# Kernel optimization log

Hardware: AMD Instinct MI355X
Metric: run time of the kernel (lower is better)

The kernel has to match this reference:

```python
import jax, jax.numpy as jnp
import numpy as np

B, S, H, L = 4096, 64, 768, 5
TEMP = 0.07
BN_EPS = 1e-5


def setup_inputs() -> dict:
    key = jax.random.key(0)
    ks = jax.random.split(key, 8)
    seq = jax.random.normal(ks[0], (B, S, H), dtype=jnp.float32)
    labels = jax.random.randint(ks[1], (B,), 0, L)
    s = 1.0 / np.sqrt(H)
    return {
        'sequence_output': seq,
        'cls_gamma': jnp.ones((H,), jnp.float32),
        'cls_beta': jnp.zeros((H,), jnp.float32),
        'cls_W': jax.random.normal(ks[2], (H, H), jnp.float32) * s,
        'cls_b': jax.random.normal(ks[3], (H,), jnp.float32) * 0.01,
        'label_gamma': jnp.ones((H,), jnp.float32),
        'label_beta': jnp.zeros((H,), jnp.float32),
        'label_W': jax.random.normal(ks[4], (H, H), jnp.float32) * s,
        'label_b': jax.random.normal(ks[5], (H,), jnp.float32) * 0.01,
        'labels': labels,
    }


def _batchnorm(x, gamma, beta):
    # training-mode BatchNorm1d: biased batch stats
    m = x.mean(0)
    v = jnp.mean((x - m) ** 2, axis=0)
    return (x - m) * jax.lax.rsqrt(v + BN_EPS) * gamma + beta


def _l2norm(x):
    return x / jnp.sqrt(jnp.sum(x * x, axis=-1, keepdims=True)).clip(1e-12)


def reference(sequence_output, cls_gamma, cls_beta, cls_W, cls_b,
              label_gamma, label_beta, label_W, label_b, labels):
    z = sequence_output[:, 0, :]  # [B,H]; dropout is identity in eval
    # label token spans: 'No relation' -> positions 1:3 (mean), rest single tokens 3..6
    theta = jnp.stack([
        sequence_output[:, 1:3, :].mean(axis=1),
        sequence_output[:, 3, :],
        sequence_output[:, 4, :],
        sequence_output[:, 5, :],
        sequence_output[:, 6, :],
    ], axis=1)  # [B,L,H]
    z_cl, theta_cl = z, theta

    zp = _batchnorm(z, cls_gamma, cls_beta) @ cls_W.T + cls_b  # [B,H]
    tp = _batchnorm(theta.reshape(-1, H), label_gamma, label_beta) @ label_W.T + label_b
    tp = tp.reshape(-1, L, H)  # [B,L,H]
    logits = jnp.einsum('blh,bh->bl', tp, zp)  # [B,L]

    # ---- dual supervised contrastive loss (vectorized over the python loops) ----
    z_norm = _l2norm(z_cl)        # [B,H]
    theta_norm = _l2norm(theta_cl)  # [B,L,H]
    same = labels[:, None] == labels[None, :]          # [B,B]
    eye = jnp.eye(labels.shape[0], dtype=bool)
    pos_mask = (same & ~eye).astype(jnp.float32)       # positives (same label, j != i)
    neg_mask = (~same).astype(jnp.float32)             # negatives (different label)
    has_pos = (same & ~eye).any(axis=1)

    # l_z: anchor z_i vs theta_j[labels_i] (pos) and all theta_j[:] for diff-label j (neg)
    expS = jnp.exp(jnp.einsum('ih,jlh->ijl', z_norm, theta_norm) / TEMP)  # [B,B,L]
    expS_at_lab = jnp.take_along_axis(
        expS, jnp.broadcast_to(labels[:, None, None], expS.shape[:2] + (1,)), axis=2
    )[..., 0]  # expS[i,j,labels[i]] -> [B,B]
    pos_z = jnp.sum(expS_at_lab * pos_mask, axis=1)
    neg_z = jnp.sum(expS.sum(axis=-1) * neg_mask, axis=1)
    l_z = jnp.where(has_pos, -jnp.log(pos_z / (pos_z + neg_z + 1e-8)), 0.0).sum()

    # l_theta: anchor theta_i[labels_i] vs z_j
    anchor_theta = jnp.take_along_axis(theta_norm, labels[:, None, None], axis=1)[:, 0, :]  # [B,H]
    expT = jnp.exp(anchor_theta @ z_norm.T / TEMP)  # [B,B]
    pos_t = jnp.sum(expT * pos_mask, axis=1)
    neg_t = jnp.sum(expT * neg_mask, axis=1)
    l_t = jnp.where(has_pos, -jnp.log(pos_t / (pos_t + neg_t + 1e-8)), 0.0).sum()

    dual_loss = (l_z + l_t) / labels.shape[0]
    return logits, dual_loss
```

## Files before the change

### kernel.cpp

```cpp
#include <hip/hip_runtime.h>
#include <hip/hip_bf16.h>
#include <cstdint>
#include <cstddef>

#define B_N 4096
#define S_N 64
#define H_N 768
#define L_N 5
#define TEMP_INV (1.0f / 0.07f)
#define BN_EPS 1e-5f

typedef __attribute__((ext_vector_type(8))) short short8;
typedef __attribute__((ext_vector_type(4))) float f32x4;

__device__ __forceinline__ void async_copy16(void* lds, const void* g) {
  __builtin_amdgcn_global_load_lds(
      (const __attribute__((address_space(1))) unsigned int*)g,
      (__attribute__((address_space(3))) unsigned int*)lds, 16, 0, 0);
}

__device__ __forceinline__ unsigned short bf16b(float x) {
  __hip_bfloat16 h = __float2bfloat16(x);
  return *reinterpret_cast<unsigned short*>(&h);
}
__device__ __forceinline__ void store_bf16x4(void* p, float4 v) {
  ushort4 o = make_ushort4(bf16b(v.x), bf16b(v.y), bf16b(v.z), bf16b(v.w));
  *reinterpret_cast<ushort4*>(p) = o;
}

__device__ inline float block_reduce_sum256(float v, float* sbuf) {
#pragma unroll
  for (int off = 32; off > 0; off >>= 1) v += __shfl_down(v, off, 64);
  int lane = threadIdx.x & 63;
  int wid = threadIdx.x >> 6;
  __syncthreads();
  if (lane == 0) sbuf[wid] = v;
  __syncthreads();
  float r = 0.f;
  if (threadIdx.x == 0) r = sbuf[0] + sbuf[1] + sbuf[2] + sbuf[3];
  return r;
}

__global__ __launch_bounds__(256) void extract_kernel(
    const float* __restrict__ seq, __hip_bfloat16* __restrict__ zb,
    __hip_bfloat16* __restrict__ tb, float* __restrict__ zn_inv,
    float* __restrict__ thn_inv, float* __restrict__ sum_z,
    float* __restrict__ ssq_z, float* __restrict__ sum_t,
    float* __restrict__ ssq_t) {
  __shared__ float pr[8][6][3];
  int t = threadIdx.x;
  int wv = t >> 6, ln = t & 63;
  bool act = t < 192;
  int c4 = t * 4;
  int b0 = blockIdx.x * 8;
  float zs[4] = {}, zq[4] = {}, ts4[4] = {}, tq4[4] = {};
  for (int r = 0; r < 8; ++r) {
    int b = b0 + r;
    const float* base = seq + (size_t)b * (S_N * H_N);
    float pv[6] = {0.f, 0.f, 0.f, 0.f, 0.f, 0.f};
    if (act) {
      float4 z4 = *(const float4*)(base + c4);
      store_bf16x4(zb + (size_t)b * H_N + c4, z4);
      pv[0] = z4.x * z4.x + z4.y * z4.y + z4.z * z4.z + z4.w * z4.w;
      zs[0] += z4.x; zs[1] += z4.y; zs[2] += z4.z; zs[3] += z4.w;
      zq[0] += z4.x * z4.x; zq[1] += z4.y * z4.y;
      zq[2] += z4.z * z4.z; zq[3] += z4.w * z4.w;
#pragma unroll
      for (int l = 0; l < L_N; ++l) {
        float4 v4;
        if (l == 0) {
          float4 a4 = *(const float4*)(base + H_N + c4);
          float4 b4 = *(const float4*)(base + 2 * H_N + c4);
          v4 = make_float4(0.5f * (a4.x + b4.x), 0.5f * (a4.y + b4.y),
                           0.5f * (a4.z + b4.z), 0.5f * (a4.w + b4.w));
        } else {
          v4 = *(const float4*)(base + (size_t)(l + 2) * H_N + c4);
        }
        store_bf16x4(tb + ((size_t)b * L_N + l) * H_N + c4, v4);
        pv[1 + l] = v4.x * v4.x + v4.y * v4.y + v4.z * v4.z + v4.w * v4.w;
        ts4[0] += v4.x; ts4[1] += v4.y; ts4[2] += v4.z; ts4[3] += v4.w;
        tq4[0] += v4.x * v4.x; tq4[1] += v4.y * v4.y;
        tq4[2] += v4.z * v4.z; tq4[3] += v4.w * v4.w;
      }
    }
#pragma unroll
    for (int v = 0; v < 6; ++v) {
      float x = pv[v];
#pragma unroll
      for (int off = 32; off > 0; off >>= 1) x += __shfl_down(x, off, 64);
      if (ln == 0 && wv < 3) pr[r][v][wv] = x;
    }
  }
  __syncthreads();
  if (t < 48) {
    int r = t / 6, v = t - r * 6;
    float s = pr[r][v][0] + pr[r][v][1] + pr[r][v][2];
    float inv = 1.f / fmaxf(sqrtf(s), 1e-12f);
    int b = b0 + r;
    if (v == 0) zn_inv[b] = inv;
    else thn_inv[b * L_N + (v - 1)] = inv;
  }
  if (act) {
#pragma unroll
    for (int j = 0; j < 4; ++j) {
      atomicAdd(&sum_z[c4 + j], zs[j]);
      atomicAdd(&ssq_z[c4 + j], zq[j]);
      atomicAdd(&sum_t[c4 + j], ts4[j]);
      atomicAdd(&ssq_t[c4 + j], tq4[j]);
    }
  }
}

__global__ void count_kernel(const int* __restrict__ labels, int* __restrict__ cnt) {
  int i = blockIdx.x * 256 + threadIdx.x;
  if (i < B_N) atomicAdd(&cnt[labels[i]], 1);
}

__global__ void finalize_kernel(
    const float* __restrict__ sum_z, const float* __restrict__ ssq_z,
    const float* __restrict__ sum_t, const float* __restrict__ ssq_t,
    const float* __restrict__ g_z, const float* __restrict__ b_z,
    const float* __restrict__ g_t, const float* __restrict__ b_t,
    float* __restrict__ sz_s, float* __restrict__ sz_t,
    float* __restrict__ st_s, float* __restrict__ st_t) {
  int h = blockIdx.x * 256 + threadIdx.x;
  if (h >= H_N) return;
  {
    float m = sum_z[h] * (1.f / B_N);
    float v = ssq_z[h] * (1.f / B_N) - m * m;
    float s = g_z[h] * rsqrtf(v + BN_EPS);
    sz_s[h] = s;
    sz_t[h] = b_z[h] - m * s;
  }
  {
    float m = sum_t[h] * (1.f / (B_N * L_N));
    float v = ssq_t[h] * (1.f / (B_N * L_N)) - m * m;
    float s = g_t[h] * rsqrtf(v + BN_EPS);
    st_s[h] = s;
    st_t[h] = b_t[h] - m * s;
  }
}

__global__ __launch_bounds__(256) void prep_cls_kernel(
    const float* __restrict__ W, const float* __restrict__ szs,
    const float* __restrict__ szt, const float* __restrict__ bias,
    __hip_bfloat16* __restrict__ Wb, float* __restrict__ cprime) {
  __shared__ float sbuf[4];
  int n = blockIdx.x;
  int t = threadIdx.x;
  float dot = 0.f;
  if (t < 192) {
    int c4 = t * 4;
    const float* row = W + (size_t)n * H_N;
    float4 w4 = *(const float4*)(row + c4);
    float4 s4 = *(const float4*)(szs + c4);
    float4 t4 = *(const float4*)(szt + c4);
    store_bf16x4(Wb + (size_t)n * H_N + c4,
                 make_float4(w4.x * s4.x, w4.y * s4.y, w4.z * s4.z, w4.w * s4.w));
    dot = w4.x * t4.x + w4.y * t4.y + w4.z * t4.z + w4.w * t4.w;
  }
  float s = block_reduce_sum256(dot, sbuf);
  if (t == 0) cprime[n] = s + bias[n];
}

__global__ __launch_bounds__(256) void transpose_wl_kernel(
    const float* __restrict__ Wl, __hip_bfloat16* __restrict__ WlT) {
  __shared__ float tile[32][33];
  int t = threadIdx.x;
  int tx = t & 31, ty0 = t >> 5;
  int n0 = blockIdx.x * 32, k0 = blockIdx.y * 32;
#pragma unroll
  for (int p = 0; p < 4; ++p)
    tile[ty0 + p * 8][tx] = Wl[(size_t)(n0 + ty0 + p * 8) * H_N + k0 + tx];
  __syncthreads();
#pragma unroll
  for (int p = 0; p < 4; ++p) {
    unsigned short us = bf16b(tile[tx][ty0 + p * 8]);
    *((unsigned short*)WlT + (size_t)(k0 + ty0 + p * 8) * H_N + n0 + tx) = us;
  }
}

template <bool WRITE_BF16, bool HAS_BIAS>
__global__ __launch_bounds__(256) void gemm128_kernel(
    const __hip_bfloat16* __restrict__ A, const __hip_bfloat16* __restrict__ Bm,
    const float* __restrict__ bias, float* __restrict__ outF,
    __hip_bfloat16* __restrict__ outB) {
  __shared__ __align__(16) __hip_bfloat16 Asm[128 * 32];
  __shared__ __align__(16) __hip_bfloat16 Bsm[128 * 32];
  int tid = threadIdx.x, lane = tid & 63, wid = tid >> 6;
  int wr = wid >> 1, wc = wid & 1;
  int i0 = blockIdx.x * 128, n0 = blockIdx.y * 128;
  int llo = lane & 15, lhi = lane >> 4;
  f32x4 acc[4][4] = {};
  for (int k0 = 0; k0 < H_N; k0 += 32) {
#pragma unroll
    for (int r = 0; r < 2; ++r) {
      int s = r * 256 + wid * 64 + lane;
      int row = s >> 2, kc = (s & 3) * 8;
      size_t go = (size_t)row * H_N + k0 + kc;
      async_copy16((char*)Asm + (size_t)(r * 256 + wid * 64) * 16,
                   A + (size_t)i0 * H_N + go);
      async_copy16((char*)Bsm + (size_t)(r * 256 + wid * 64) * 16,
                   Bm + (size_t)n0 * H_N + go);
    }
    __syncthreads();
    short8 a[4], b[4];
#pragma unroll
    for (int m = 0; m < 4; ++m)
      a[m] = *(const short8*)((const char*)Asm +
                              ((wr * 64 + m * 16 + llo) * 32 + lhi * 8) * 2);
#pragma unroll
    for (int n = 0; n < 4; ++n)
      b[n] = *(const short8*)((const char*)Bsm +
                              ((wc * 64 + n * 16 + llo) * 32 + lhi * 8) * 2);
#pragma unroll
    for (int m = 0; m < 4; ++m)
#pragma unroll
      for (int n = 0; n < 4; ++n)
        acc[m][n] =
            __builtin_amdgcn_mfma_f32_16x16x32_bf16(a[m], b[n], acc[m][n], 0, 0, 0);
    __syncthreads();
  }
#pragma unroll
  for (int n = 0; n < 4; ++n) {
    int col = n0 + wc * 64 + n * 16 + llo;
    float bv = HAS_BIAS ? bias[col] : 0.f;
#pragma unroll
    for (int m = 0; m < 4; ++m) {
#pragma unroll
      for (int r = 0; r < 4; ++r) {
        int row = i0 + wr * 64 + m * 16 + lhi * 4 + r;
        float val = acc[m][n][r] + bv;
        outF[(size_t)row * H_N + col] = val;
        if (WRITE_BF16)
          outB[(size_t)row * H_N + col] = __float2bfloat16(val);
      }
    }
  }
}

__global__ __launch_bounds__(256) void logits_kernel(
    const float* __restrict__ seq, const float* __restrict__ u,
    const float* __restrict__ zp, const float* __restrict__ st_s,
    const float* __restrict__ st_t, const float* __restrict__ label_b,
    float* __restrict__ out) {
  __shared__ float sbuf[4];
  int b = blockIdx.x;
  int t = threadIdx.x;
  bool act = t < 192;
  int c4 = t * 4;
  float4 w4 = make_float4(0.f, 0.f, 0.f, 0.f);
  float apart = 0.f;
  if (act) {
    float4 u4 = *(const float4*)(u + (size_t)b * H_N + c4);
    float4 zp4 = *(const float4*)(zp + (size_t)b * H_N + c4);
    float4 ss4 = *(const float4*)(st_s + c4);
    float4 tt4 = *(const float4*)(st_t + c4);
    float4 lb4 = *(const float4*)(label_b + c4);
    w4 = make_float4(u4.x * ss4.x, u4.y * ss4.y, u4.z * ss4.z, u4.w * ss4.w);
    apart = u4.x * tt4.x + u4.y * tt4.y + u4.z * tt4.z + u4.w * tt4.w +
            zp4.x * lb4.x + zp4.y * lb4.y + zp4.z * lb4.z + zp4.w * lb4.w;
  }
  float alpha = block_reduce_sum256(apart, sbuf);
  const float* base = seq + (size_t)b * (S_N * H_N);
#pragma unroll
  for (int l = 0; l < L_N; ++l) {
    float part = 0.f;
    if (act) {
      float4 v4;
      if (l == 0) {
        float4 a4 = *(const float4*)(base + H_N + c4);
        float4 b4 = *(const float4*)(base + 2 * H_N + c4);
        v4 = make_float4(0.5f * (a4.x + b4.x), 0.5f * (a4.y + b4.y),
                         0.5f * (a4.z + b4.z), 0.5f * (a4.w + b4.w));
      } else {
        v4 = *(const float4*)(base + (size_t)(l + 2) * H_N + c4);
      }
      part = v4.x * w4.x + v4.y * w4.y + v4.z * w4.z + v4.w * w4.w;
    }
    float s = block_reduce_sum256(part, sbuf);
    if (t == 0) out[b * L_N + l] = s + alpha;
  }
}

#define NT_K 24
__global__ __launch_bounds__(256, 3) void sgemm_fused_kernel(
    const __hip_bfloat16* __restrict__ zb, const __hip_bfloat16* __restrict__ tb,
    const float* __restrict__ zn_inv, const float* __restrict__ thn_inv,
    const int* __restrict__ labels, float* __restrict__ pos_z,
    float* __restrict__ neg_z, float* __restrict__ pos_t,
    float* __restrict__ neg_t) {
  __shared__ __align__(128) char ldsbuf[2][16384];

  const int tid = threadIdx.x;
  const int lane = tid & 63, wid = tid >> 6;
  const int llo = lane & 15, lhi = lane >> 4;
  const int wr = wid >> 1, wc = wid & 1;
  const int xcd = blockIdx.x & 7;
  const int s0 = blockIdx.x >> 3;
  const int i0 = (xcd * 4 + (s0 & 3)) * 128;
  const int n0 = (s0 >> 2) * 128;

  f32x4 acc[4][4] = {};

  auto stage = [&](int c, int kt) {
#pragma unroll
    for (int h = 0; h < 2; ++h) {
      int s = h * 256 + tid;
      int R = s >> 3, sp = s & 7;
      int l = sp ^ (R & 7);
      int grow = 2 * R + (l >> 2);
      int gk = kt * 32 + (l & 3) * 8;
      int wub = (h * 256 + wid * 64) * 16;
      async_copy16(&ldsbuf[c][0] + wub, zb + (size_t)(i0 + grow) * H_N + gk);
      async_copy16(&ldsbuf[c][8192] + wub, tb + (size_t)(n0 + grow) * H_N + gk);
    }
  };

  auto fragOff = [&](int r) {
    int R = r >> 1;
    int slot = (r & 1) * 4 + lhi;
    return R * 128 + ((slot ^ (R & 7)) * 16);
  };

  stage(0, 0);
  asm volatile("s_waitcnt vmcnt(0)" ::: "memory");
  __builtin_amdgcn_s_barrier();

  for (int t = 0; t < NT_K; ++t) {
    if (t + 1 < NT_K) stage((t + 1) & 1, t + 1);
    const char* A = &ldsbuf[t & 1][0];
    const char* B = &ldsbuf[t & 1][8192];
    short8 a[4], b[4];
#pragma unroll
    for (int m = 0; m < 4; ++m) a[m] = *(const short8*)(A + fragOff(wr * 64 + m * 16 + llo));
#pragma unroll
    for (int n = 0; n < 4; ++n) b[n] = *(const short8*)(B + fragOff(wc * 64 + n * 16 + llo));
    asm volatile("s_waitcnt lgkmcnt(0)" ::: "memory");
    __builtin_amdgcn_sched_barrier(0);
    __builtin_amdgcn_s_setprio(1);
#pragma unroll
    for (int m = 0; m < 4; ++m)
#pragma unroll
      for (int n = 0; n < 4; ++n)
        acc[m][n] =
            __builtin_amdgcn_mfma_f32_16x16x32_bf16(a[m], b[n], acc[m][n], 0, 0, 0);
    __builtin_amdgcn_s_setprio(0);
    asm volatile("s_waitcnt vmcnt(0)" ::: "memory");
    __builtin_amdgcn_s_barrier();
  }
  __syncthreads();

  float* rpos = (float*)&ldsbuf[0][0];
  float* rneg = rpos + 128;
  float* cpos = rneg + 128;
  float* cneg = cpos + 128;
  float* rnorm = cneg + 128;
  float* cnorm = rnorm + 128;
  int* rowlab = (int*)(cnorm + 128);
  int* colj = rowlab + 128;
  int* coll = colj + 128;
  int* collab = coll + 128;

  if (tid < 128) {
    rowlab[tid] = labels[i0 + tid];
    rnorm[tid] = zn_inv[i0 + tid] * TEMP_INV;
    int c = n0 + tid;
    int j = c / 5;
    colj[tid] = j;
    coll[tid] = c - j * 5;
    collab[tid] = labels[j];
    cnorm[tid] = thn_inv[c];
    rpos[tid] = 0.f; rneg[tid] = 0.f; cpos[tid] = 0.f; cneg[tid] = 0.f;
  }
  __syncthreads();

  int cl[4], jg[4], lv[4], lj[4];
  float cs[4];
#pragma unroll
  for (int ni = 0; ni < 4; ++ni) {
    cl[ni] = wc * 64 + ni * 16 + llo;
    jg[ni] = colj[cl[ni]];
    lv[ni] = coll[cl[ni]];
    lj[ni] = collab[cl[ni]];
    cs[ni] = cnorm[cl[ni]];
  }
  float cpAcc[4] = {}, cnAcc[4] = {};
#pragma unroll
  for (int mi = 0; mi < 4; ++mi) {
#pragma unroll
    for (int r = 0; r < 4; ++r) {
      int rl = wr * 64 + mi * 16 + lhi * 4 + r;
      int ig = i0 + rl;
      int li = rowlab[rl];
      float rscale = rnorm[rl];
      float rp = 0.f, rn = 0.f;
#pragma unroll
      for (int ni = 0; ni < 4; ++ni) {
        float e = __expf(acc[mi][ni][r] * rscale * cs[ni]);
        bool same = (li == lj[ni]);
        bool diag = (ig == jg[ni]);
        if (same) {
          if (!diag && lv[ni] == li) { rp += e; cpAcc[ni] += e; }
        } else {
          rn += e;
          if (lv[ni] == lj[ni]) cnAcc[ni] += e;
        }
      }
      if (rp != 0.f) atomicAdd(&rpos[rl], rp);
      if (rn != 0.f) atomicAdd(&rneg[rl], rn);
    }
  }
#pragma unroll
  for (int ni = 0; ni < 4; ++ni) {
    if (cpAcc[ni] != 0.f) atomicAdd(&cpos[cl[ni]], cpAcc[ni]);
    if (cnAcc[ni] != 0.f) atomicAdd(&cneg[cl[ni]], cnAcc[ni]);
  }
  __syncthreads();
  if (tid < 128) {
    float v;
    v = rpos[tid]; if (v != 0.f) atomicAdd(&pos_z[i0 + tid], v);
    v = rneg[tid]; if (v != 0.f) atomicAdd(&neg_z[i0 + tid], v);
    int j = colj[tid];
    v = cpos[tid]; if (v != 0.f) atomicAdd(&pos_t[j], v);
    v = cneg[tid]; if (v != 0.f) atomicAdd(&neg_t[j], v);
  }
}

__global__ __launch_bounds__(256) void loss_kernel(
    const float* __restrict__ pos_z, const float* __restrict__ neg_z,
    const float* __restrict__ pos_t, const float* __restrict__ neg_t,
    const int* __restrict__ labels, const int* __restrict__ cnt,
    float* __restrict__ out_loss) {
  __shared__ float sbuf[4];
  int i = blockIdx.x * 256 + threadIdx.x;
  float term = 0.f;
  int li = labels[i];
  if (cnt[li] > 1) {
    float pz = pos_z[i], nz = neg_z[i];
    float pt = pos_t[i], nt = neg_t[i];
    term = -logf(pz / (pz + nz + 1e-8f)) - logf(pt / (pt + nt + 1e-8f));
  }
  float s = block_reduce_sum256(term, sbuf);
  if (threadIdx.x == 0) atomicAdd(out_loss, s * (1.0f / B_N));
}

extern "C" void kernel_launch(void* const* d_in, const int* in_sizes, int n_in,
                              void* d_out, int out_size, void* d_ws, size_t ws_size,
                              hipStream_t stream) {
  const float* seq = (const float*)d_in[0];
  const float* cls_gamma = (const float*)d_in[1];
  const float* cls_beta = (const float*)d_in[2];
  const float* cls_W = (const float*)d_in[3];
  const float* cls_b = (const float*)d_in[4];
  const float* label_gamma = (const float*)d_in[5];
  const float* label_beta = (const float*)d_in[6];
  const float* label_W = (const float*)d_in[7];
  const float* label_b = (const float*)d_in[8];
  const int* labels = (const int*)d_in[9];
  float* out = (float*)d_out;
  float* ws = (float*)d_ws;

  constexpr size_t OFF_SUMZ = 0;
  constexpr size_t OFF_SSQZ = 768;
  constexpr size_t OFF_SUMT = 1536;
  constexpr size_t OFF_SSQT = 2304;
  constexpr size_t OFF_POSZ = 3072;
  constexpr size_t OFF_NEGZ = 7168;
  constexpr size_t OFF_POST = 11264;
  constexpr size_t OFF_NEGT = 15360;
  constexpr size_t OFF_CNT = 19456;
  constexpr size_t ZERO_FLOATS = 19464;
  constexpr size_t OFF_SZS = 19464;
  constexpr size_t OFF_SZT = 20232;
  constexpr size_t OFF_STS = 21000;
  constexpr size_t OFF_STT = 21768;
  constexpr size_t OFF_ZNI = 22536;
  constexpr size_t OFF_TNI = 26632;
  constexpr size_t OFF_CPRIME = 47112;
  constexpr size_t OFF_ZP = 47880;
  constexpr size_t OFF_U = OFF_ZP + (size_t)B_N * H_N;
  constexpr size_t F32_END = OFF_U + (size_t)B_N * H_N;
  constexpr size_t BYTE_ZB = F32_END * sizeof(float);
  constexpr size_t BYTE_TB = BYTE_ZB + (size_t)B_N * H_N * 2;
  constexpr size_t BYTE_ZPB = BYTE_TB + (size_t)B_N * L_N * H_N * 2;
  constexpr size_t BYTE_WCB = BYTE_ZPB + (size_t)B_N * H_N * 2;
  constexpr size_t BYTE_WLT = BYTE_WCB + (size_t)H_N * H_N * 2;
  constexpr size_t TOTAL_BYTES = BYTE_WLT + (size_t)H_N * H_N * 2;
  if (ws_size < TOTAL_BYTES) return;

  __hip_bfloat16* zb = (__hip_bfloat16*)((char*)d_ws + BYTE_ZB);
  __hip_bfloat16* tb = (__hip_bfloat16*)((char*)d_ws + BYTE_TB);
  __hip_bfloat16* zpb = (__hip_bfloat16*)((char*)d_ws + BYTE_ZPB);
  __hip_bfloat16* wcb = (__hip_bfloat16*)((char*)d_ws + BYTE_WCB);
  __hip_bfloat16* wlt = (__hip_bfloat16*)((char*)d_ws + BYTE_WLT);

  hipMemsetAsync(d_ws, 0, ZERO_FLOATS * sizeof(float), stream);
  hipMemsetAsync((char*)d_out + (size_t)B_N * L_N * sizeof(float), 0, sizeof(float),
                 stream);

  extract_kernel<<<512, 256, 0, stream>>>(seq, zb, tb, ws + OFF_ZNI, ws + OFF_TNI,
                                          ws + OFF_SUMZ, ws + OFF_SSQZ,
                                          ws + OFF_SUMT, ws + OFF_SSQT);
  count_kernel<<<16, 256, 0, stream>>>(labels, (int*)(ws + OFF_CNT));
  finalize_kernel<<<3, 256, 0, stream>>>(
      ws + OFF_SUMZ, ws + OFF_SSQZ, ws + OFF_SUMT, ws + OFF_SSQT, cls_gamma,
      cls_beta, label_gamma, label_beta, ws + OFF_SZS, ws + OFF_SZT, ws + OFF_STS,
      ws + OFF_STT);
  prep_cls_kernel<<<H_N, 256, 0, stream>>>(cls_W, ws + OFF_SZS, ws + OFF_SZT, cls_b,
                                           wcb, ws + OFF_CPRIME);
  transpose_wl_kernel<<<dim3(24, 24), 256, 0, stream>>>(label_W, wlt);
  gemm128_kernel<true, true><<<dim3(32, 6), 256, 0, stream>>>(
      zb, wcb, ws + OFF_CPRIME, ws + OFF_ZP, zpb);
  gemm128_kernel<false, false><<<dim3(32, 6), 256, 0, stream>>>(
      zpb, wlt, nullptr, ws + OFF_U, nullptr);
  logits_kernel<<<B_N, 256, 0, stream>>>(seq, ws + OFF_U, ws + OFF_ZP, ws + OFF_STS,
                                         ws + OFF_STT, label_b, out);
  sgemm_fused_kernel<<<5120, 256, 0, stream>>>(
      zb, tb, ws + OFF_ZNI, ws + OFF_TNI, labels, ws + OFF_POSZ, ws + OFF_NEGZ,
      ws + OFF_POST, ws + OFF_NEGT);
  loss_kernel<<<16, 256, 0, stream>>>(ws + OFF_POSZ, ws + OFF_NEGZ, ws + OFF_POST,
                                      ws + OFF_NEGT, labels,
                                      (const int*)(ws + OFF_CNT),
                                      out + (size_t)B_N * L_N);
}
```

Baseline: 461.1 us.

## Load GEMM fragments directly from global into registers, dropping LDS staging

The bf16 similarity GEMM no longer stages tiles in LDS through async global-to-LDS copies with barriers. Each wave now loads its MFMA fragments straight from global memory into registers, double-buffered across two k-steps, and LDS is kept only for the small epilogue arrays. This removes the LDS round trip and the per-iteration barriers. In exchange, every wave re-fetches rows that other waves in the block also read, which raises global/L2 traffic, and the 16-byte loads per row are less coalesced.

```diff
diff --git a/kernel.cpp b/kernel.cpp
--- a/kernel.cpp
+++ b/kernel.cpp
@@ -290,7 +290,9 @@
     const int* __restrict__ labels, float* __restrict__ pos_z,
     float* __restrict__ neg_z, float* __restrict__ pos_t,
     float* __restrict__ neg_t) {
-  __shared__ __align__(128) char ldsbuf[2][16384];
+  __shared__ float rpos[128], rneg[128], cpos[128], cneg[128];
+  __shared__ float rnorm[128], cnorm[128];
+  __shared__ int rowlab[128], colj[128], coll[128], collab[128];
 
   const int tid = threadIdx.x;
   const int lane = tid & 63, wid = tid >> 6;
@@ -301,66 +303,47 @@
   const int i0 = (xcd * 4 + (s0 & 3)) * 128;
   const int n0 = (s0 >> 2) * 128;
 
+  const __hip_bfloat16* pa = zb + (size_t)(i0 + wr * 64 + llo) * H_N + lhi * 8;
+  const __hip_bfloat16* pb = tb + (size_t)(n0 + wc * 64 + llo) * H_N + lhi * 8;
+
   f32x4 acc[4][4] = {};
-
-  auto stage = [&](int c, int kt) {
-#pragma unroll
-    for (int h = 0; h < 2; ++h) {
-      int s = h * 256 + tid;
-      int R = s >> 3, sp = s & 7;
-      int l = sp ^ (R & 7);
-      int grow = 2 * R + (l >> 2);
-      int gk = kt * 32 + (l & 3) * 8;
-      int wub = (h * 256 + wid * 64) * 16;
-      async_copy16(&ldsbuf[c][0] + wub, zb + (size_t)(i0 + grow) * H_N + gk);
-      async_copy16(&ldsbuf[c][8192] + wub, tb + (size_t)(n0 + grow) * H_N + gk);
-    }
-  };
-
-  auto fragOff = [&](int r) {
-    int R = r >> 1;
-    int slot = (r & 1) * 4 + lhi;
-    return R * 128 + ((slot ^ (R & 7)) * 16);
-  };
-
-  stage(0, 0);
-  asm volatile("s_waitcnt vmcnt(0)" ::: "memory");
-  __builtin_amdgcn_s_barrier();
-
-  for (int t = 0; t < NT_K; ++t) {
-    if (t + 1 < NT_K) stage((t + 1) & 1, t + 1);
-    const char* A = &ldsbuf[t & 1][0];
-    const char* B = &ldsbuf[t & 1][8192];
-    short8 a[4], b[4];
-#pragma unroll
-    for (int m = 0; m < 4; ++m) a[m] = *(const short8*)(A + fragOff(wr * 64 + m * 16 + llo));
-#pragma unroll
-    for (int n = 0; n < 4; ++n) b[n] = *(const short8*)(B + fragOff(wc * 64 + n * 16 + llo));
-    asm volatile("s_waitcnt lgkmcnt(0)" ::: "memory");
-    __builtin_amdgcn_sched_barrier(0);
+  short8 a0[4], b0[4], a1[4], b1[4];
+
+#pragma unroll
+  for (int m = 0; m < 4; ++m) a0[m] = *(const short8*)(pa + m * 16 * H_N);
+#pragma unroll
+  for (int n = 0; n < 4; ++n) b0[n] = *(const short8*)(pb + n * 16 * H_N);
+
+  for (int t = 0; t < NT_K; t += 2) {
+    const int k1 = (t + 1) * 32;
+#pragma unroll
+    for (int m = 0; m < 4; ++m) a1[m] = *(const short8*)(pa + m * 16 * H_N + k1);
+#pragma unroll
+    for (int n = 0; n < 4; ++n) b1[n] = *(const short8*)(pb + n * 16 * H_N + k1);
     __builtin_amdgcn_s_setprio(1);
 #pragma unroll
     for (int m = 0; m < 4; ++m)
 #pragma unroll
       for (int n = 0; n < 4; ++n)
         acc[m][n] =
-            __builtin_amdgcn_mfma_f32_16x16x32_bf16(a[m], b[n], acc[m][n], 0, 0, 0);
+            __builtin_amdgcn_mfma_f32_16x16x32_bf16(a0[m], b0[n], acc[m][n], 0, 0, 0);
     __builtin_amdgcn_s_setprio(0);
-    asm volatile("s_waitcnt vmcnt(0)" ::: "memory");
-    __builtin_amdgcn_s_barrier();
-  }
-  __syncthreads();
-
-  float* rpos = (float*)&ldsbuf[0][0];
-  float* rneg = rpos + 128;
-  float* cpos = rneg + 128;
-  float* cneg = cpos + 128;
-  float* rnorm = cneg + 128;
-  float* cnorm = rnorm + 128;
-  int* rowlab = (int*)(cnorm + 128);
-  int* colj = rowlab + 128;
-  int* coll = colj + 128;
-  int* collab = coll + 128;
+    if (t + 2 < NT_K) {
+      const int k2 = (t + 2) * 32;
+#pragma unroll
+      for (int m = 0; m < 4; ++m) a0[m] = *(const short8*)(pa + m * 16 * H_N + k2);
+#pragma unroll
+      for (int n = 0; n < 4; ++n) b0[n] = *(const short8*)(pb + n * 16 * H_N + k2);
+    }
+    __builtin_amdgcn_s_setprio(1);
+#pragma unroll
+    for (int m = 0; m < 4; ++m)
+#pragma unroll
+      for (int n = 0; n < 4; ++n)
+        acc[m][n] =
+            __builtin_amdgcn_mfma_f32_16x16x32_bf16(a1[m], b1[n], acc[m][n], 0, 0, 0);
+    __builtin_amdgcn_s_setprio(0);
+  }
 
   if (tid < 128) {
     rowlab[tid] = labels[i0 + tid];
```

Measured after the change: 629.1 us. +36.4%, slower.

## Per-wave private LDS staging in contrastive GEMM, reuse bf16 theta in logits, fuse label count

Applied to the files above, without the earlier changes.

The fused contrastive GEMM now gives each wave its own LDS region holding only its 64-row A and B slices, triple-staged two tiles ahead. Each wave waits only on its own loads with vmcnt, so the per-iteration block barriers go away. LDS use doubles to 64KB and the occupancy hint of 3 is dropped, which may lower occupancy, and each wave now loads redundant copies of data its neighbours also load. Separately, logits reads the bf16 theta buffer instead of re-reading fp32 sequence rows, and the label-count kernel is folded into extract; the bf16 read slightly lowers logits precision.

```diff
diff --git a/kernel.cpp b/kernel.cpp
--- a/kernel.cpp
+++ b/kernel.cpp
@@ -27,6 +27,10 @@
   ushort4 o = make_ushort4(bf16b(v.x), bf16b(v.y), bf16b(v.z), bf16b(v.w));
   *reinterpret_cast<ushort4*>(p) = o;
 }
+__device__ __forceinline__ float bf2f(unsigned short u) {
+  unsigned int x = ((unsigned int)u) << 16;
+  return *reinterpret_cast<float*>(&x);
+}
 
 __device__ inline float block_reduce_sum256(float v, float* sbuf) {
 #pragma unroll
@@ -46,13 +50,15 @@
     __hip_bfloat16* __restrict__ tb, float* __restrict__ zn_inv,
     float* __restrict__ thn_inv, float* __restrict__ sum_z,
     float* __restrict__ ssq_z, float* __restrict__ sum_t,
-    float* __restrict__ ssq_t) {
+    float* __restrict__ ssq_t, const int* __restrict__ labels,
+    int* __restrict__ cnt) {
   __shared__ float pr[8][6][3];
   int t = threadIdx.x;
   int wv = t >> 6, ln = t & 63;
   bool act = t < 192;
   int c4 = t * 4;
   int b0 = blockIdx.x * 8;
+  if (t < 8) atomicAdd(&cnt[labels[b0 + t]], 1);
   float zs[4] = {}, zq[4] = {}, ts4[4] = {}, tq4[4] = {};
   for (int r = 0; r < 8; ++r) {
     int b = b0 + r;
@@ -109,11 +115,6 @@
       atomicAdd(&ssq_t[c4 + j], tq4[j]);
     }
   }
-}
-
-__global__ void count_kernel(const int* __restrict__ labels, int* __restrict__ cnt) {
-  int i = blockIdx.x * 256 + threadIdx.x;
-  if (i < B_N) atomicAdd(&cnt[labels[i]], 1);
 }
 
 __global__ void finalize_kernel(
@@ -240,7 +241,7 @@
 }
 
 __global__ __launch_bounds__(256) void logits_kernel(
-    const float* __restrict__ seq, const float* __restrict__ u,
+    const __hip_bfloat16* __restrict__ tb, const float* __restrict__ u,
     const float* __restrict__ zp, const float* __restrict__ st_s,
     const float* __restrict__ st_t, const float* __restrict__ label_b,
     float* __restrict__ out) {
@@ -262,21 +263,14 @@
             zp4.x * lb4.x + zp4.y * lb4.y + zp4.z * lb4.z + zp4.w * lb4.w;
   }
   float alpha = block_reduce_sum256(apart, sbuf);
-  const float* base = seq + (size_t)b * (S_N * H_N);
 #pragma unroll
   for (int l = 0; l < L_N; ++l) {
     float part = 0.f;
     if (act) {
-      float4 v4;
-      if (l == 0) {
-        float4 a4 = *(const float4*)(base + H_N + c4);
-        float4 b4 = *(const float4*)(base + 2 * H_N + c4);
-        v4 = make_float4(0.5f * (a4.x + b4.x), 0.5f * (a4.y + b4.y),
-                         0.5f * (a4.z + b4.z), 0.5f * (a4.w + b4.w));
-      } else {
-        v4 = *(const float4*)(base + (size_t)(l + 2) * H_N + c4);
-      }
-      part = v4.x * w4.x + v4.y * w4.y + v4.z * w4.z + v4.w * w4.w;
+      ushort4 tv = *(const ushort4*)((const unsigned short*)tb +
+                                     ((size_t)b * L_N + l) * H_N + c4);
+      part = bf2f(tv.x) * w4.x + bf2f(tv.y) * w4.y + bf2f(tv.z) * w4.z +
+             bf2f(tv.w) * w4.w;
     }
     float s = block_reduce_sum256(part, sbuf);
     if (t == 0) out[b * L_N + l] = s + alpha;
@@ -284,13 +278,13 @@
 }
 
 #define NT_K 24
-__global__ __launch_bounds__(256, 3) void sgemm_fused_kernel(
+__global__ __launch_bounds__(256) void sgemm_fused_kernel(
     const __hip_bfloat16* __restrict__ zb, const __hip_bfloat16* __restrict__ tb,
     const float* __restrict__ zn_inv, const float* __restrict__ thn_inv,
     const int* __restrict__ labels, float* __restrict__ pos_z,
     float* __restrict__ neg_z, float* __restrict__ pos_t,
     float* __restrict__ neg_t) {
-  __shared__ __align__(128) char ldsbuf[2][16384];
+  __shared__ __align__(128) char ldsbuf[4][16384];
 
   const int tid = threadIdx.x;
   const int lane = tid & 63, wid = tid >> 6;
@@ -301,19 +295,32 @@
   const int i0 = (xcd * 4 + (s0 & 3)) * 128;
   const int n0 = (s0 >> 2) * 128;
 
+  char* wbase = &ldsbuf[wid][0];
+  const __hip_bfloat16* srcA = zb + (size_t)(i0 + wr * 64) * H_N;
+  const __hip_bfloat16* srcB = tb + (size_t)(n0 + wc * 64) * H_N;
+
   f32x4 acc[4][4] = {};
 
   auto stage = [&](int c, int kt) {
-#pragma unroll
-    for (int h = 0; h < 2; ++h) {
-      int s = h * 256 + tid;
+    char* dA = wbase + c * 8192;
+    char* dB = dA + 4096;
+#pragma unroll
+    for (int i = 0; i < 4; ++i) {
+      int s = i * 64 + lane;
       int R = s >> 3, sp = s & 7;
       int l = sp ^ (R & 7);
       int grow = 2 * R + (l >> 2);
       int gk = kt * 32 + (l & 3) * 8;
-      int wub = (h * 256 + wid * 64) * 16;
-      async_copy16(&ldsbuf[c][0] + wub, zb + (size_t)(i0 + grow) * H_N + gk);
-      async_copy16(&ldsbuf[c][8192] + wub, tb + (size_t)(n0 + grow) * H_N + gk);
+      async_copy16(dA + i * 1024, srcA + (size_t)grow * H_N + gk);
+    }
+#pragma unroll
+    for (int i = 0; i < 4; ++i) {
+      int s = i * 64 + lane;
+      int R = s >> 3, sp = s & 7;
+      int l = sp ^ (R & 7);
+      int grow = 2 * R + (l >> 2);
+      int gk = kt * 32 + (l & 3) * 8;
+      async_copy16(dB + i * 1024, srcB + (size_t)grow * H_N + gk);
     }
   };
 
@@ -324,20 +331,22 @@
   };
 
   stage(0, 0);
-  asm volatile("s_waitcnt vmcnt(0)" ::: "memory");
-  __builtin_amdgcn_s_barrier();
-
+  stage(1, 1);
   for (int t = 0; t < NT_K; ++t) {
-    if (t + 1 < NT_K) stage((t + 1) & 1, t + 1);
-    const char* A = &ldsbuf[t & 1][0];
-    const char* B = &ldsbuf[t & 1][8192];
+    if (t < NT_K - 1)
+      asm volatile("s_waitcnt vmcnt(8)" ::: "memory");
+    else
+      asm volatile("s_waitcnt vmcnt(0)" ::: "memory");
+    const char* A = wbase + (t & 1) * 8192;
+    const char* B = A + 4096;
     short8 a[4], b[4];
 #pragma unroll
-    for (int m = 0; m < 4; ++m) a[m] = *(const short8*)(A + fragOff(wr * 64 + m * 16 + llo));
-#pragma unroll
-    for (int n = 0; n < 4; ++n) b[n] = *(const short8*)(B + fragOff(wc * 64 + n * 16 + llo));
+    for (int m = 0; m < 4; ++m) a[m] = *(const short8*)(A + fragOff(m * 16 + llo));
+#pragma unroll
+    for (int n = 0; n < 4; ++n) b[n] = *(const short8*)(B + fragOff(n * 16 + llo));
     asm volatile("s_waitcnt lgkmcnt(0)" ::: "memory");
     __builtin_amdgcn_sched_barrier(0);
+    if (t + 2 < NT_K) stage(t & 1, t + 2);
     __builtin_amdgcn_s_setprio(1);
 #pragma unroll
     for (int m = 0; m < 4; ++m)
@@ -346,8 +355,6 @@
         acc[m][n] =
             __builtin_amdgcn_mfma_f32_16x16x32_bf16(a[m], b[n], acc[m][n], 0, 0, 0);
     __builtin_amdgcn_s_setprio(0);
-    asm volatile("s_waitcnt vmcnt(0)" ::: "memory");
-    __builtin_amdgcn_s_barrier();
   }
   __syncthreads();
 
@@ -501,8 +508,8 @@
 
   extract_kernel<<<512, 256, 0, stream>>>(seq, zb, tb, ws + OFF_ZNI, ws + OFF_TNI,
                                           ws + OFF_SUMZ, ws + OFF_SSQZ,
-                                          ws + OFF_SUMT, ws + OFF_SSQT);
-  count_kernel<<<16, 256, 0, stream>>>(labels, (int*)(ws + OFF_CNT));
+                                          ws + OFF_SUMT, ws + OFF_SSQT, labels,
+                                          (int*)(ws + OFF_CNT));
   finalize_kernel<<<3, 256, 0, stream>>>(
       ws + OFF_SUMZ, ws + OFF_SSQZ, ws + OFF_SUMT, ws + OFF_SSQT, cls_gamma,
       cls_beta, label_gamma, label_beta, ws + OFF_SZS, ws + OFF_SZT, ws + OFF_STS,
@@ -514,7 +521,7 @@
       zb, wcb, ws + OFF_CPRIME, ws + OFF_ZP, zpb);
   gemm128_kernel<false, false><<<dim3(32, 6), 256, 0, stream>>>(
       zpb, wlt, nullptr, ws + OFF_U, nullptr);
-  logits_kernel<<<B_N, 256, 0, stream>>>(seq, ws + OFF_U, ws + OFF_ZP, ws + OFF_STS,
+  logits_kernel<<<B_N, 256, 0, stream>>>(tb, ws + OFF_U, ws + OFF_ZP, ws + OFF_STS,
                                          ws + OFF_STT, label_b, out);
   sgemm_fused_kernel<<<5120, 256, 0, stream>>>(
       zb, tb, ws + OFF_ZNI, ws + OFF_TNI, labels, ws + OFF_POSZ, ws + OFF_NEGZ,
```

Result: slower. 522.2 us (+13.2%).
